# Kernel tuning notes

Measured on AMD Instinct MI355X. Metric: run time of the kernel, lower is better.

The kernel has to match this reference:

```python
import jax, jax.numpy as jnp
import numpy as np

MAX_DIS = 4  # max_displacement == pad_size


def setup_inputs() -> dict:
    key = jax.random.key(0)
    k1, k2 = jax.random.split(key)
    in1 = jax.random.normal(k1, (2, 64, 32, 32, 32), dtype=jnp.float32)
    in2 = jax.random.normal(k2, (2, 64, 32, 32, 32), dtype=jnp.float32)
    return {"in1": in1, "in2": in2}


def _corr3d(in1, in2, max_dis):
    # in1, in2: [B, C, H, W, D]
    B, C, H, W, D = in1.shape
    K = 2 * max_dis + 1
    pad = ((0, 0), (0, 0), (max_dis, max_dis), (max_dis, max_dis), (max_dis, max_dis))
    in2_pad = jnp.pad(in2, pad)  # [B, C, H+2m, W+2m, D+2m]
    # gather index for the depth axis: all K shifted windows at once
    idx_d = jnp.arange(K)[:, None] + jnp.arange(D)[None, :]  # [K, D]
    outs = []
    # loop over the (dy, dx) shift grid (fixed 9x9 structural loop);
    # the dz shifts and the channel reduction are fully vectorized.
    for dy in range(K):
        for dx in range(K):
            s = in2_pad[:, :, dy:dy + H, dx:dx + W, :]          # [B, C, H, W, D+2m]
            w = s[..., idx_d]                                   # [B, C, H, W, K, D]
            # sum over channels -> K correlation channels (dz inner)
            outs.append(jnp.einsum('bchwkd,bchwd->bkhwd', w, in1))
    # channel order matches torch: n = dy*K*K + dx*K + dz
    return jnp.concatenate(outs, axis=1)  # [B, K^3, H, W, D]


def reference(in1, in2):
    return _corr3d(in1, in2, MAX_DIS)
```

## Files before the change

kernel.cpp:

```cpp
#include <hip/hip_runtime.h>

typedef __fp16 h2 __attribute__((ext_vector_type(2)));
typedef __fp16 h8 __attribute__((ext_vector_type(8)));
typedef float f4 __attribute__((ext_vector_type(4)));

namespace {
constexpr int JSTR = 72;
constexpr int JN = 48;
constexpr int COLH = JN * JSTR;
}

__global__ __launch_bounds__(256, 4) void corr3d_mfma(
    const float* __restrict__ in1, const float* __restrict__ in2,
    float* __restrict__ out)
{
  __shared__ __align__(16) __fp16 colbuf[2][COLH];
  __shared__ __align__(16) float obuf[2][2 * 9 * 32];

  const int tid = threadIdx.x;
  const int blk = ((blockIdx.x & 7) << 7) | (blockIdx.x >> 3);
  const int b = blk >> 9;
  const int h = (blk >> 4) & 31;
  const int w0 = (blk & 15) << 1;

  const int lane = tid & 63;
  const int wv = tid >> 6;
  const int jb = (wv == 0) ? 0 : (wv == 3) ? 32 : 16;
  const int db = (wv >= 2) ? 16 : 0;
  const int l15 = lane & 15;
  const int lhi = lane >> 4;

  const float* in1b = in1 + ((size_t)b << 21);
  const float* in2b = in2 + ((size_t)b << 21);

  for (int i = tid; i < 1152; i += 256) {
    const int bu = i / 576;
    const int r = i - bu * 576;
    const int jrow = r / 36;
    const int cc = r - jrow * 36;
    const int j = (jrow < 4) ? jrow : jrow + 32;
    h2 z = {(__fp16)0.f, (__fp16)0.f};
    *(h2*)&colbuf[bu][j * JSTR + cc * 2] = z;
  }

  const int sd = tid & 31;
  const int scq = tid >> 5;

  auto stage = [&](const float* src, bool valid, __fp16* dst) {
#pragma unroll
    for (int it = 0; it < 4; ++it) {
      const int cp = scq + (it << 3);
      h2 v = {(__fp16)0.f, (__fp16)0.f};
      if (valid) {
        const float x = src[((size_t)(2 * cp) << 15) + sd];
        const float y = src[((size_t)(2 * cp + 1) << 15) + sd];
        v = __builtin_amdgcn_cvt_pkrtz(x, y);
      }
      *(h2*)&dst[(4 + sd) * JSTR + 2 * cp] = v;
    }
  };

  h8 bfr[2][2];
#pragma unroll
  for (int pos = 0; pos < 2; ++pos) {
    __syncthreads();
    stage(in1b + (h << 10) + ((w0 + pos) << 5), true, colbuf[0]);
    __syncthreads();
#pragma unroll
    for (int ch = 0; ch < 2; ++ch)
      bfr[pos][ch] =
          *(const h8*)&colbuf[0][(4 + db + l15) * JSTR + ch * 32 + (lhi << 3)];
  }
  __syncthreads();
  {
    const int hp = h - 4, wp = w0 - 4;
    const bool valid = ((unsigned)hp < 32u) && ((unsigned)wp < 32u);
    stage(in2b + (hp << 10) + (wp << 5), valid, colbuf[0]);
  }
  __syncthreads();

  int boff[4];
  unsigned bmask = 0;
#pragma unroll
  for (int r = 0; r < 4; ++r) {
    const int m = (lhi << 2) + r;
    const int dz = jb + m - db - l15;
    if ((unsigned)dz < 9u) bmask |= 1u << r;
    boff[r] = dz * 32 + db + l15;
  }

  for (int ci = 0; ci < 90; ++ci) {
    float lx[4], ly[4];
    bool nvalid = false;
    if (ci + 1 < 90) {
      const int cn = ci + 1;
      const int hcn = cn / 10;
      const int wcn = cn - hcn * 10;
      const int hp = h - 4 + hcn;
      const int wp = w0 - 4 + wcn;
      nvalid = ((unsigned)hp < 32u) && ((unsigned)wp < 32u);
      if (nvalid) {
        const float* src = in2b + (hp << 10) + (wp << 5);
#pragma unroll
        for (int it = 0; it < 4; ++it) {
          const int cp = scq + (it << 3);
          lx[it] = src[((size_t)(2 * cp) << 15) + sd];
          ly[it] = src[((size_t)(2 * cp + 1) << 15) + sd];
        }
      }
    }

    const int hc = ci / 10;
    const int wc = ci - hc * 10;
    const bool serve[2] = {wc <= 8, wc >= 1};

    const __fp16* cb = colbuf[ci & 1];
    float* ob = obuf[ci & 1];
    const h8 a0 = *(const h8*)&cb[(jb + l15) * JSTR + (lhi << 3)];
    const h8 a1 = *(const h8*)&cb[(jb + l15) * JSTR + 32 + (lhi << 3)];
#pragma unroll
    for (int pos = 0; pos < 2; ++pos) {
      if (serve[pos]) {
        f4 acc = {0.f, 0.f, 0.f, 0.f};
        acc = __builtin_amdgcn_mfma_f32_16x16x32_f16(a0, bfr[pos][0], acc, 0, 0, 0);
        acc = __builtin_amdgcn_mfma_f32_16x16x32_f16(a1, bfr[pos][1], acc, 0, 0, 0);
#pragma unroll
        for (int r = 0; r < 4; ++r)
          if (bmask & (1u << r)) ob[pos * 288 + boff[r]] = acc[r];
      }
    }

    if (ci > 0 && tid < 144) {
      const int cprev = ci - 1;
      const int hcp = cprev / 10;
      const int wcp = cprev - hcp * 10;
      const int pos = tid >= 72;
      const int rr = tid - pos * 72;
      const int dz = rr >> 3;
      const int q = rr & 7;
      const bool sv = pos ? (wcp >= 1) : (wcp <= 8);
      if (sv) {
        const f4 v = *(const f4*)&obuf[cprev & 1][pos * 288 + dz * 32 + (q << 2)];
        const size_t ch = (size_t)(b * 729 + (hcp * 9 + (wcp - pos)) * 9 + dz);
        f4* dstp = (f4*)(out + (ch << 15) + (h << 10) + ((w0 + pos) << 5) + (q << 2));
        __builtin_nontemporal_store(v, dstp);
      }
    }

    if (ci + 1 < 90) {
#pragma unroll
      for (int it = 0; it < 4; ++it) {
        const int cp = scq + (it << 3);
        h2 v = {(__fp16)0.f, (__fp16)0.f};
        if (nvalid) v = __builtin_amdgcn_cvt_pkrtz(lx[it], ly[it]);
        *(h2*)&colbuf[(ci + 1) & 1][(4 + sd) * JSTR + 2 * cp] = v;
      }
    }

    __syncthreads();
  }

  if (tid >= 72 && tid < 144) {
    const int rr = tid - 72;
    const int dz = rr >> 3;
    const int q = rr & 7;
    const f4 v = *(const f4*)&obuf[1][288 + dz * 32 + (q << 2)];
    const size_t ch = (size_t)(b * 729 + (8 * 9 + 8) * 9 + dz);
    f4* dstp = (f4*)(out + (ch << 15) + (h << 10) + ((w0 + 1) << 5) + (q << 2));
    __builtin_nontemporal_store(v, dstp);
  }
}

extern "C" void kernel_launch(void* const* d_in, const int* in_sizes, int n_in,
                              void* d_out, int out_size, void* d_ws, size_t ws_size,
                              hipStream_t stream) {
  const float* in1 = (const float*)d_in[0];
  const float* in2 = (const float*)d_in[1];
  float* out = (float*)d_out;
  corr3d_mfma<<<dim3(1024), dim3(256), 0, stream>>>(in1, in2, out);
}
```

Before: 279.9 us.

## Split the displacement loop across two blocks to double grid size

Each block now handles half of the 90 (dy,dx) column iterations, and the grid doubles to 2048 blocks. The launch-bounds occupancy hint rises from 4 to 8 blocks per CU. The block-index swizzle, the initial in2 staging and the final output flush are adjusted for the split range. The aim is more parallelism and latency hiding on a chip with many CUs. In exchange, the in1 staging and prologue are duplicated per half, and register pressure may be tighter under the higher occupancy bound.

```diff
diff --git a/kernel.cpp b/kernel.cpp
--- a/kernel.cpp
+++ b/kernel.cpp
@@ -10,7 +10,7 @@
 constexpr int COLH = JN * JSTR;
 }
 
-__global__ __launch_bounds__(256, 4) void corr3d_mfma(
+__global__ __launch_bounds__(256, 8) void corr3d_mfma(
     const float* __restrict__ in1, const float* __restrict__ in2,
     float* __restrict__ out)
 {
@@ -18,10 +18,13 @@
   __shared__ __align__(16) float obuf[2][2 * 9 * 32];
 
   const int tid = threadIdx.x;
-  const int blk = ((blockIdx.x & 7) << 7) | (blockIdx.x >> 3);
-  const int b = blk >> 9;
-  const int h = (blk >> 4) & 31;
-  const int w0 = (blk & 15) << 1;
+  const int blk = ((blockIdx.x & 7) << 8) | (blockIdx.x >> 3);
+  const int half = blk & 1;
+  const int w0 = ((blk >> 1) & 15) << 1;
+  const int h = (blk >> 5) & 31;
+  const int b = blk >> 10;
+  const int ciLo = half ? 45 : 0;
+  const int ciHi = half ? 90 : 45;
 
   const int lane = tid & 63;
   const int wv = tid >> 6;
@@ -73,9 +76,11 @@
   }
   __syncthreads();
   {
-    const int hp = h - 4, wp = w0 - 4;
+    const int hcn = ciLo / 10;
+    const int wcn = ciLo - hcn * 10;
+    const int hp = h - 4 + hcn, wp = w0 - 4 + wcn;
     const bool valid = ((unsigned)hp < 32u) && ((unsigned)wp < 32u);
-    stage(in2b + (hp << 10) + (wp << 5), valid, colbuf[0]);
+    stage(in2b + (hp << 10) + (wp << 5), valid, colbuf[ciLo & 1]);
   }
   __syncthreads();
 
@@ -89,10 +94,10 @@
     boff[r] = dz * 32 + db + l15;
   }
 
-  for (int ci = 0; ci < 90; ++ci) {
+  for (int ci = ciLo; ci < ciHi; ++ci) {
     float lx[4], ly[4];
     bool nvalid = false;
-    if (ci + 1 < 90) {
+    if (ci + 1 < ciHi) {
       const int cn = ci + 1;
       const int hcn = cn / 10;
       const int wcn = cn - hcn * 10;
@@ -130,7 +135,7 @@
       }
     }
 
-    if (ci > 0 && tid < 144) {
+    if (ci > ciLo && tid < 144) {
       const int cprev = ci - 1;
       const int hcp = cprev / 10;
       const int wcp = cprev - hcp * 10;
@@ -147,7 +152,7 @@
       }
     }
 
-    if (ci + 1 < 90) {
+    if (ci + 1 < ciHi) {
 #pragma unroll
       for (int it = 0; it < 4; ++it) {
         const int cp = scq + (it << 3);
@@ -160,14 +165,23 @@
     __syncthreads();
   }
 
-  if (tid >= 72 && tid < 144) {
-    const int rr = tid - 72;
-    const int dz = rr >> 3;
-    const int q = rr & 7;
-    const f4 v = *(const f4*)&obuf[1][288 + dz * 32 + (q << 2)];
-    const size_t ch = (size_t)(b * 729 + (8 * 9 + 8) * 9 + dz);
-    f4* dstp = (f4*)(out + (ch << 15) + (h << 10) + ((w0 + 1) << 5) + (q << 2));
-    __builtin_nontemporal_store(v, dstp);
+  {
+    const int cl = ciHi - 1;
+    const int hcp = cl / 10;
+    const int wcp = cl - hcp * 10;
+    if (tid < 144) {
+      const int pos = tid >= 72;
+      const int rr = tid - pos * 72;
+      const int dz = rr >> 3;
+      const int q = rr & 7;
+      const bool sv = pos ? (wcp >= 1) : (wcp <= 8);
+      if (sv) {
+        const f4 v = *(const f4*)&obuf[cl & 1][pos * 288 + dz * 32 + (q << 2)];
+        const size_t ch = (size_t)(b * 729 + (hcp * 9 + (wcp - pos)) * 9 + dz);
+        f4* dstp = (f4*)(out + (ch << 15) + (h << 10) + ((w0 + pos) << 5) + (q << 2));
+        __builtin_nontemporal_store(v, dstp);
+      }
+    }
   }
 }
 
@@ -177,5 +191,5 @@
   const float* in1 = (const float*)d_in[0];
   const float* in2 = (const float*)d_in[1];
   float* out = (float*)d_out;
-  corr3d_mfma<<<dim3(1024), dim3(256), 0, stream>>>(in1, in2, out);
+  corr3d_mfma<<<dim3(2048), dim3(256), 0, stream>>>(in1, in2, out);
 }
```

After: 253.3 us. 9.5% less time.
